# Kernel optimization log

Measured on AMD Instinct MI355X. Metric: run time of the kernel, lower is better.

## Reference

```python
import jax, jax.numpy as jnp
import numpy as np

BATCH, SEQ, DIM = 8, 2048, 512
NUM_Q, CODEBOOK = 8, 1024


def setup_inputs() -> dict:
    key = jax.random.key(0)
    k1, k2 = jax.random.split(key)
    x = jax.random.normal(k1, (BATCH, SEQ, DIM), dtype=jnp.float32)
    # one codebook per quantizer (uniform codebook size -> stacked [q, c, d])
    codebooks = jax.random.normal(k2, (NUM_Q, CODEBOOK, DIM), dtype=jnp.float32)
    return {"x": x, "codebooks": codebooks}


def reference(x, codebooks):
    """Residual VQ (Algorithm 1, SoundStream). Sequential nearest-neighbor
    quantization of the residual with straight-through estimator.
    project_in/project_out are Identity (codebook_dim == dim).
    Returns (quantized_out [b,n,d], indices [b,n,q], commit_losses [q]).
    """
    residual = x
    quantized_out = jnp.zeros_like(x)
    all_indices = []
    all_losses = []
    num_q = codebooks.shape[0]
    for q in range(num_q):  # small fixed loop over quantizer layers
        cb = codebooks[q]  # [c, d]
        # argmin of squared euclidean distance; ||r||^2 is constant over codes
        scores = -2.0 * jnp.einsum('bnd,cd->bnc', residual, cb) \
                 + jnp.sum(cb * cb, axis=-1)  # [b, n, c]
        idx = jnp.argmin(scores, axis=-1)  # [b, n]
        quant = cb[idx]  # gather codes: [b, n, d]
        # commitment loss (mse of detached quantize vs layer input)
        commit = jnp.mean((jax.lax.stop_gradient(quant) - residual) ** 2)
        # straight-through estimator
        quant_st = residual + jax.lax.stop_gradient(quant - residual)
        quantized_out = quantized_out + quant_st
        residual = residual - jax.lax.stop_gradient(quant)
        all_indices.append(idx)
        all_losses.append(commit)
    indices = jnp.stack(all_indices, axis=-1)  # [b, n, q]
    losses = jnp.stack(all_losses)  # [q]
    return quantized_out, indices, losses
```

## Files before the change

kernel.cpp:

```cpp
#include <hip/hip_runtime.h>
#include <cstdint>
#include <cstddef>


#define BATCH 8
#define SEQ   2048
#define DIM   512
#define NUMQ  8
#define CODES 1024
#define NPTS  (BATCH*SEQ)
#define MPTS  64
#define NWG   (NPTS/MPTS)
#define NTHR  512
#define NCHUNK 32
#define NCHUNK_TOT (NUMQ*NCHUNK)
#define CHUNK_BYTES 32768

#define OUT_IDX   (BATCH*SEQ*DIM)
#define OUT_LOSS  (OUT_IDX + BATCH*SEQ*NUMQ)

#define WS_LOSS   0
#define WS_CNORM  1024
#define WS_CBH    40960

typedef _Float16 f16x8  __attribute__((ext_vector_type(8)));
typedef _Float16 f16x4  __attribute__((ext_vector_type(4)));
typedef float    f32x16 __attribute__((ext_vector_type(16)));

__global__ void k_zero(double* loss) {
  if (threadIdx.x < NUMQ) loss[threadIdx.x] = 0.0;
}

__global__ void k_cnorm(const float* __restrict__ cb, float* __restrict__ cnorm) {
  int r = blockIdx.x * blockDim.x + threadIdx.x;
  const float* row = cb + (size_t)r * DIM;
  float s = 0.f;
  for (int d = 0; d < DIM; d += 4) {
    float4 v = *(const float4*)(row + d);
    s += v.x * v.x + v.y * v.y + v.z * v.z + v.w * v.w;
  }
  cnorm[r] = s;
}

__global__ void k_prep(const float* __restrict__ cb, unsigned char* __restrict__ cbH) {
  unsigned u = blockIdx.x * blockDim.x + threadIdx.x;
  unsigned h  = u & 1;
  unsigned v  = u >> 1;
  unsigned c  = v & 127;
  unsigned g  = (v >> 7) & 1;
  unsigned w  = (v >> 8) & 7;
  unsigned ks = (v >> 11) & 31;
  unsigned q  = v >> 16;
  unsigned code = (w << 7) | c;
  unsigned k = ks * 16 + g * 8 + h * 4;
  float4 val = *(const float4*)(cb + ((size_t)((q << 10) | code)) * DIM + k);
  f16x4 o;
  o[0] = (_Float16)val.x; o[1] = (_Float16)val.y;
  o[2] = (_Float16)val.z; o[3] = (_Float16)val.w;
  *(f16x4*)(cbH + (size_t)u * 8) = o;
}

__device__ __forceinline__ void stage(const unsigned char* __restrict__ cbH, int n,
                                      unsigned char* slot, int w, int cl) {
  const unsigned char* src = cbH + (size_t)n * CHUNK_BYTES + (w << 12) + (cl << 4);
  #pragma unroll
  for (int i = 0; i < 4; ++i)
    __builtin_amdgcn_global_load_lds(
        (const __attribute__((address_space(1))) void*)(src + i * 1024),
        (__attribute__((address_space(3))) void*)(slot + i * 1024), 16, 0, 0);
}

__launch_bounds__(NTHR, 2)
__global__ void k_main(const float* __restrict__ x, const float* __restrict__ cb,
                       const unsigned char* __restrict__ cbH,
                       const float* __restrict__ cnorm,
                       double* __restrict__ lossAcc,
                       float* __restrict__ out)
{
  __shared__ __align__(16) unsigned char Af[MPTS * DIM * 2];
  __shared__ __align__(16) unsigned char Bs[8][2][4096];
  __shared__ float          s1w[MPTS][8];
  __shared__ unsigned short id1w[MPTS][8];
  __shared__ unsigned short cand[MPTS][8][4];
  __shared__ unsigned char  ccnt[MPTS][8];
  __shared__ float          gmA[MPTS];
  __shared__ int            win0A[MPTS];
  __shared__ unsigned short idxs[MPTS][NUMQ];
  __shared__ double         lred[8];

  const int tid = threadIdx.x;
  const int cl  = tid & 63;
  const int w   = tid >> 6;
  const int l31 = cl & 31;
  const int l5  = cl >> 5;
  const int wg  = blockIdx.x;

  const int rp = tid >> 3;
  const int rj = tid & 7;
  const size_t gp = (size_t)wg * MPTS + rp;
  float4 r4[16];
  {
    const float4* xr = (const float4*)(x + gp * DIM + rj * 64);
    #pragma unroll
    for (int i = 0; i < 16; ++i) r4[i] = xr[i];
  }

  unsigned char* mySlot = &Bs[w][0][0];
  const int bOff = l5 * 2048 + l31 * 16;

  stage(cbH, 0, mySlot, w, cl);
  stage(cbH, 1, mySlot + 4096, w, cl);

  for (int q = 0; q < NUMQ; ++q) {
    #pragma unroll
    for (int i = 0; i < 8; ++i) {
      float4 a = r4[2 * i], b = r4[2 * i + 1];
      f16x8 v;
      v[0] = (_Float16)a.x; v[1] = (_Float16)a.y; v[2] = (_Float16)a.z; v[3] = (_Float16)a.w;
      v[4] = (_Float16)b.x; v[5] = (_Float16)b.y; v[6] = (_Float16)b.z; v[7] = (_Float16)b.w;
      int sl = ((i << 3) | rj) ^ (rp & 31);
      *(f16x8*)(Af + rp * 1024 + (sl << 4)) = v;
    }
    __syncthreads();

    f32x16 acc[2][4];
    #pragma unroll
    for (int mt = 0; mt < 2; ++mt)
      #pragma unroll
      for (int nt = 0; nt < 4; ++nt)
        #pragma unroll
        for (int e = 0; e < 16; ++e) acc[mt][nt][e] = 0.0f;

    #pragma unroll 1
    for (int ks = 0; ks < NCHUNK; ++ks) {
      if (q == NUMQ - 1 && ks == NCHUNK - 1)
        asm volatile("s_waitcnt vmcnt(0)" ::: "memory");
      else
        asm volatile("s_waitcnt vmcnt(4)" ::: "memory");
      const unsigned char* bufp = mySlot + ((ks & 1) << 12);
      const int s5 = (ks << 1) | l5;
      const int sf = ((((s5 & 7) << 3) | (s5 >> 3)) ^ l31) << 4;
      f16x8 a0 = *(const f16x8*)(Af + l31 * 1024 + sf);
      f16x8 a1 = *(const f16x8*)(Af + 32768 + l31 * 1024 + sf);
      f16x8 b0 = *(const f16x8*)(bufp + bOff);
      f16x8 b1 = *(const f16x8*)(bufp + bOff + 512);
      f16x8 b2 = *(const f16x8*)(bufp + bOff + 1024);
      f16x8 b3 = *(const f16x8*)(bufp + bOff + 1536);
      __builtin_amdgcn_s_setprio(1);
      acc[0][0] = __builtin_amdgcn_mfma_f32_32x32x16_f16(a0, b0, acc[0][0], 0, 0, 0);
      acc[0][1] = __builtin_amdgcn_mfma_f32_32x32x16_f16(a0, b1, acc[0][1], 0, 0, 0);
      acc[0][2] = __builtin_amdgcn_mfma_f32_32x32x16_f16(a0, b2, acc[0][2], 0, 0, 0);
      acc[0][3] = __builtin_amdgcn_mfma_f32_32x32x16_f16(a0, b3, acc[0][3], 0, 0, 0);
      acc[1][0] = __builtin_amdgcn_mfma_f32_32x32x16_f16(a1, b0, acc[1][0], 0, 0, 0);
      acc[1][1] = __builtin_amdgcn_mfma_f32_32x32x16_f16(a1, b1, acc[1][1], 0, 0, 0);
      acc[1][2] = __builtin_amdgcn_mfma_f32_32x32x16_f16(a1, b2, acc[1][2], 0, 0, 0);
      acc[1][3] = __builtin_amdgcn_mfma_f32_32x32x16_f16(a1, b3, acc[1][3], 0, 0, 0);
      __builtin_amdgcn_s_setprio(0);
      asm volatile("s_waitcnt lgkmcnt(0)" ::: "memory");
      const int n = (q << 5) + ks + 2;
      if (n < NCHUNK_TOT) stage(cbH, n, mySlot + ((ks & 1) << 12), w, cl);
    }

    {
      const float* cnq = cnorm + (q << 10) + (w << 7) + l31;
      const float cn0 = cnq[0], cn1 = cnq[32], cn2 = cnq[64], cn3 = cnq[96];
      #pragma unroll
      for (int mt = 0; mt < 2; ++mt) {
        acc[mt][0] = acc[mt][0] * -2.0f + cn0;
        acc[mt][1] = acc[mt][1] * -2.0f + cn1;
        acc[mt][2] = acc[mt][2] * -2.0f + cn2;
        acc[mt][3] = acc[mt][3] * -2.0f + cn3;
      }
    }

    #pragma unroll
    for (int mt = 0; mt < 2; ++mt)
      #pragma unroll
      for (int r = 0; r < 16; ++r) {
        float s = acc[mt][0][r]; int bi = l31;
        if (acc[mt][1][r] < s) { s = acc[mt][1][r]; bi = 32 + l31; }
        if (acc[mt][2][r] < s) { s = acc[mt][2][r]; bi = 64 + l31; }
        if (acc[mt][3][r] < s) { s = acc[mt][3][r]; bi = 96 + l31; }
        #pragma unroll
        for (int m = 1; m < 32; m <<= 1) {
          float os = __shfl_xor(s, m); int ob = __shfl_xor(bi, m);
          if (os < s || (os == s && ob < bi)) { s = os; bi = ob; }
        }
        if (l31 == 0) {
          int p = mt * 32 + (r & 3) + 8 * (r >> 2) + 4 * l5;
          s1w[p][w] = s; id1w[p][w] = (unsigned short)bi;
        }
      }
    __syncthreads();

    if (tid < MPTS) {
      int p = tid;
      float bs = s1w[p][0]; int bi = id1w[p][0];
      #pragma unroll
      for (int ww = 1; ww < 8; ++ww) {
        float s = s1w[p][ww];
        if (s < bs) { bs = s; bi = ww * 128 + id1w[p][ww]; }
      }
      gmA[p] = bs; win0A[p] = bi;
    }
    __syncthreads();

    #pragma unroll
    for (int mt = 0; mt < 2; ++mt)
      #pragma unroll
      for (int r = 0; r < 16; ++r) {
        const int p0 = mt * 32 + (r & 3) + 8 * (r >> 2);
        const float g0 = gmA[p0], g1 = gmA[p0 + 4];
        const float lim0 = g0 + 1.5f + 1e-4f * fabsf(g0);
        const float lim1 = g1 + 1.5f + 1e-4f * fabsf(g1);
        const float lim = l5 ? lim1 : lim0;
        unsigned long long b0 = __ballot(acc[mt][0][r] <= lim);
        unsigned long long b1 = __ballot(acc[mt][1][r] <= lim);
        unsigned long long b2 = __ballot(acc[mt][2][r] <= lim);
        unsigned long long b3 = __ballot(acc[mt][3][r] <= lim);
        if (cl == 0 || cl == 32) {
          const int p = p0 + (cl >> 3);
          unsigned short* cd = &cand[p][w][0];
          unsigned m0 = (cl == 0) ? (unsigned)b0 : (unsigned)(b0 >> 32);
          unsigned m1 = (cl == 0) ? (unsigned)b1 : (unsigned)(b1 >> 32);
          unsigned m2 = (cl == 0) ? (unsigned)b2 : (unsigned)(b2 >> 32);
          unsigned m3 = (cl == 0) ? (unsigned)b3 : (unsigned)(b3 >> 32);
          int n = 0;
          while (m0 && n < 4) { int bt = __builtin_ctz(m0); m0 &= m0 - 1; cd[n++] = (unsigned short)(bt); }
          while (m1 && n < 4) { int bt = __builtin_ctz(m1); m1 &= m1 - 1; cd[n++] = (unsigned short)(32 + bt); }
          while (m2 && n < 4) { int bt = __builtin_ctz(m2); m2 &= m2 - 1; cd[n++] = (unsigned short)(64 + bt); }
          while (m3 && n < 4) { int bt = __builtin_ctz(m3); m3 &= m3 - 1; cd[n++] = (unsigned short)(96 + bt); }
          ccnt[p][w] = (unsigned char)n;
        }
      }
    __syncthreads();

    #pragma unroll 1
    for (int pp = 0; pp < 8; ++pp) {
      const int p = (w << 3) + pp;
      int tot = 0;
      #pragma unroll
      for (int ww = 0; ww < 8; ++ww) tot += ccnt[p][ww];
      int winner;
      if (tot <= 1) {
        winner = win0A[p];
      } else {
        const size_t gpp = (size_t)wg * MPTS + p;
        double bs = 1.0e300, bs2 = 1.0e300; int bi = 0x7FFFFFFF;
        #pragma unroll 1
        for (int ww = 0; ww < 8; ++ww) {
          const int nn = ccnt[p][ww];
          #pragma unroll 1
          for (int si = 0; si < nn; ++si) {
            const int cc = ww * 128 + cand[p][ww][si];
            const float4* cr = (const float4*)(cb + ((size_t)q * CODES + cc) * DIM + (cl & 7) * 64);
            double dt = 0.0, cs = 0.0;
            #pragma unroll
            for (int i = 0; i < 16; ++i) {
              float4 cv = cr[i];
              dt += (double)r4[i].x * cv.x + (double)r4[i].y * cv.y
                  + (double)r4[i].z * cv.z + (double)r4[i].w * cv.w;
              cs += (double)cv.x * cv.x + (double)cv.y * cv.y
                  + (double)cv.z * cv.z + (double)cv.w * cv.w;
            }
            #pragma unroll
            for (int m = 1; m < 8; m <<= 1) { dt += __shfl_xor(dt, m); cs += __shfl_xor(cs, m); }
            double dtb = __shfl(dt, pp * 8), csb = __shfl(cs, pp * 8);
            double s = -2.0 * dtb + csb;
            if (s < bs) { bs2 = bs; bs = s; bi = cc; }
            else if (s < bs2) { bs2 = s; }
          }
        }
        if (bs2 - bs <= 1e-3 + 1e-6 * fabs(bs)) {
          bs = 1.0e300; bi = 0x7FFFFFFF;
          const float4* xr2 = (const float4*)(x + gpp * DIM + (cl & 7) * 64);
          #pragma unroll 1
          for (int ww = 0; ww < 8; ++ww) {
            const int nn = ccnt[p][ww];
            #pragma unroll 1
            for (int si = 0; si < nn; ++si) {
              const int cc = ww * 128 + cand[p][ww][si];
              const float4* cr = (const float4*)(cb + ((size_t)q * CODES + cc) * DIM + (cl & 7) * 64);
              double dt = 0.0, cs = 0.0;
              #pragma unroll 1
              for (int i = 0; i < 16; ++i) {
                float4 xv = xr2[i];
                double rhx = xv.x, rhy = xv.y, rhz = xv.z, rhw = xv.w;
                #pragma unroll 1
                for (int t2 = 0; t2 < q; ++t2) {
                  const float4* qr = (const float4*)(cb + ((size_t)t2 * CODES + idxs[p][t2]) * DIM + (cl & 7) * 64);
                  float4 qv = qr[i];
                  rhx -= (double)qv.x; rhy -= (double)qv.y;
                  rhz -= (double)qv.z; rhw -= (double)qv.w;
                }
                float4 cv = cr[i];
                dt += rhx * cv.x + rhy * cv.y + rhz * cv.z + rhw * cv.w;
                cs += (double)cv.x * cv.x + (double)cv.y * cv.y
                    + (double)cv.z * cv.z + (double)cv.w * cv.w;
              }
              #pragma unroll
              for (int m = 1; m < 8; m <<= 1) { dt += __shfl_xor(dt, m); cs += __shfl_xor(cs, m); }
              double dtb = __shfl(dt, pp * 8), csb = __shfl(cs, pp * 8);
              double s = -2.0 * dtb + csb;
              if (s < bs || (s == bs && cc < bi)) { bs = s; bi = cc; }
            }
          }
        }
        winner = bi;
      }
      if (cl == 0) idxs[p][q] = (unsigned short)winner;
    }
    __syncthreads();

    {
      const int win = idxs[rp][q];
      const float4* cr = (const float4*)(cb + ((size_t)q * CODES + win) * DIM + rj * 64);
      double ls = 0.0;
      #pragma unroll
      for (int i = 0; i < 16; ++i) {
        float4 cv = cr[i];
        float dx = cv.x - r4[i].x, dy = cv.y - r4[i].y;
        float dz = cv.z - r4[i].z, dw = cv.w - r4[i].w;
        ls += (double)dx * dx + (double)dy * dy + (double)dz * dz + (double)dw * dw;
        r4[i].x -= cv.x; r4[i].y -= cv.y; r4[i].z -= cv.z; r4[i].w -= cv.w;
      }
      #pragma unroll
      for (int m = 1; m < 64; m <<= 1) ls += __shfl_xor(ls, m);
      if (cl == 0) lred[w] = ls;
      __syncthreads();
      if (tid == 0) {
        double t = lred[0] + lred[1] + lred[2] + lred[3]
                 + lred[4] + lred[5] + lred[6] + lred[7];
        atomicAdd(lossAcc + q, t);
      }
      __syncthreads();
    }
  }

  {
    const float4* xr = (const float4*)(x + gp * DIM + rj * 64);
    float4* orow = (float4*)(out + gp * DIM + rj * 64);
    #pragma unroll
    for (int i = 0; i < 16; ++i) {
      float4 xv = xr[i];
      float4 o;
      o.x = xv.x - r4[i].x; o.y = xv.y - r4[i].y;
      o.z = xv.z - r4[i].z; o.w = xv.w - r4[i].w;
      orow[i] = o;
    }
  }
  if (tid < MPTS) {
    float* ob = out + OUT_IDX + ((size_t)wg * MPTS + tid) * NUMQ;
    #pragma unroll
    for (int j = 0; j < NUMQ; ++j) ob[j] = (float)idxs[tid][j];
  }
}

__global__ void k_fin(const double* __restrict__ loss, float* __restrict__ out) {
  int t = threadIdx.x;
  if (t < NUMQ)
    out[OUT_LOSS + t] = (float)(loss[t] / (double)((size_t)BATCH * SEQ * DIM));
}

extern "C" void kernel_launch(void* const* d_in, const int* in_sizes, int n_in,
                              void* d_out, int out_size, void* d_ws, size_t ws_size,
                              hipStream_t stream) {
  (void)in_sizes; (void)n_in; (void)out_size; (void)ws_size;
  const float* x  = (const float*)d_in[0];
  const float* cb = (const float*)d_in[1];
  float* out = (float*)d_out;
  char* ws = (char*)d_ws;
  double* loss = (double*)(ws + WS_LOSS);
  float* cnorm = (float*)(ws + WS_CNORM);
  unsigned char* cbH = (unsigned char*)(ws + WS_CBH);

  k_zero<<<1, 64, 0, stream>>>(loss);
  k_cnorm<<<NUMQ * CODES / 256, 256, 0, stream>>>(cb, cnorm);
  k_prep<<<NUMQ * NCHUNK * CHUNK_BYTES / 8 / 256, 256, 0, stream>>>(cb, cbH);
  k_main<<<NWG, NTHR, 0, stream>>>(x, cb, cbH, cnorm, loss, out);
  k_fin<<<1, 64, 0, stream>>>(loss, out);
}
```

Baseline: 632.1 us.

## Halve points per workgroup, single-buffer codebook chunks, raise occupancy to four blocks

```diff
diff --git a/kernel.cpp b/kernel.cpp
--- a/kernel.cpp
+++ b/kernel.cpp
@@ -9,7 +9,7 @@
 #define NUMQ  8
 #define CODES 1024
 #define NPTS  (BATCH*SEQ)
-#define MPTS  64
+#define MPTS  32
 #define NWG   (NPTS/MPTS)
 #define NTHR  512
 #define NCHUNK 32
@@ -70,7 +70,7 @@
         (__attribute__((address_space(3))) void*)(slot + i * 1024), 16, 0, 0);
 }
 
-__launch_bounds__(NTHR, 2)
+__launch_bounds__(NTHR, 4)
 __global__ void k_main(const float* __restrict__ x, const float* __restrict__ cb,
                        const unsigned char* __restrict__ cbH,
                        const float* __restrict__ cnorm,
@@ -78,7 +78,7 @@
                        float* __restrict__ out)
 {
   __shared__ __align__(16) unsigned char Af[MPTS * DIM * 2];
-  __shared__ __align__(16) unsigned char Bs[8][2][4096];
+  __shared__ __align__(16) unsigned char Bs[8][4096];
   __shared__ float          s1w[MPTS][8];
   __shared__ unsigned short id1w[MPTS][8];
   __shared__ unsigned short cand[MPTS][8][4];
@@ -95,102 +95,86 @@
   const int l5  = cl >> 5;
   const int wg  = blockIdx.x;
 
-  const int rp = tid >> 3;
-  const int rj = tid & 7;
+  const int rp = tid >> 4;
+  const int rj = tid & 15;
   const size_t gp = (size_t)wg * MPTS + rp;
-  float4 r4[16];
+  float4 r4[8];
   {
-    const float4* xr = (const float4*)(x + gp * DIM + rj * 64);
-    #pragma unroll
-    for (int i = 0; i < 16; ++i) r4[i] = xr[i];
-  }
-
-  unsigned char* mySlot = &Bs[w][0][0];
+    const float4* xr = (const float4*)(x + gp * DIM + rj * 32);
+    #pragma unroll
+    for (int i = 0; i < 8; ++i) r4[i] = xr[i];
+  }
+
+  unsigned char* mySlot = &Bs[w][0];
   const int bOff = l5 * 2048 + l31 * 16;
 
   stage(cbH, 0, mySlot, w, cl);
-  stage(cbH, 1, mySlot + 4096, w, cl);
 
   for (int q = 0; q < NUMQ; ++q) {
     #pragma unroll
-    for (int i = 0; i < 8; ++i) {
+    for (int i = 0; i < 4; ++i) {
       float4 a = r4[2 * i], b = r4[2 * i + 1];
       f16x8 v;
       v[0] = (_Float16)a.x; v[1] = (_Float16)a.y; v[2] = (_Float16)a.z; v[3] = (_Float16)a.w;
       v[4] = (_Float16)b.x; v[5] = (_Float16)b.y; v[6] = (_Float16)b.z; v[7] = (_Float16)b.w;
-      int sl = ((i << 3) | rj) ^ (rp & 31);
+      const int s = rj * 4 + i;
+      const int sl = (((s & 7) << 3) | (s >> 3)) ^ (rp & 31);
       *(f16x8*)(Af + rp * 1024 + (sl << 4)) = v;
     }
     __syncthreads();
 
-    f32x16 acc[2][4];
-    #pragma unroll
-    for (int mt = 0; mt < 2; ++mt)
-      #pragma unroll
-      for (int nt = 0; nt < 4; ++nt)
-        #pragma unroll
-        for (int e = 0; e < 16; ++e) acc[mt][nt][e] = 0.0f;
+    f32x16 acc[4];
+    #pragma unroll
+    for (int nt = 0; nt < 4; ++nt)
+      #pragma unroll
+      for (int e = 0; e < 16; ++e) acc[nt][e] = 0.0f;
 
     #pragma unroll 1
     for (int ks = 0; ks < NCHUNK; ++ks) {
-      if (q == NUMQ - 1 && ks == NCHUNK - 1)
-        asm volatile("s_waitcnt vmcnt(0)" ::: "memory");
-      else
-        asm volatile("s_waitcnt vmcnt(4)" ::: "memory");
-      const unsigned char* bufp = mySlot + ((ks & 1) << 12);
+      asm volatile("s_waitcnt vmcnt(0)" ::: "memory");
       const int s5 = (ks << 1) | l5;
       const int sf = ((((s5 & 7) << 3) | (s5 >> 3)) ^ l31) << 4;
       f16x8 a0 = *(const f16x8*)(Af + l31 * 1024 + sf);
-      f16x8 a1 = *(const f16x8*)(Af + 32768 + l31 * 1024 + sf);
-      f16x8 b0 = *(const f16x8*)(bufp + bOff);
-      f16x8 b1 = *(const f16x8*)(bufp + bOff + 512);
-      f16x8 b2 = *(const f16x8*)(bufp + bOff + 1024);
-      f16x8 b3 = *(const f16x8*)(bufp + bOff + 1536);
+      f16x8 b0 = *(const f16x8*)(mySlot + bOff);
+      f16x8 b1 = *(const f16x8*)(mySlot + bOff + 512);
+      f16x8 b2 = *(const f16x8*)(mySlot + bOff + 1024);
+      f16x8 b3 = *(const f16x8*)(mySlot + bOff + 1536);
       __builtin_amdgcn_s_setprio(1);
-      acc[0][0] = __builtin_amdgcn_mfma_f32_32x32x16_f16(a0, b0, acc[0][0], 0, 0, 0);
-      acc[0][1] = __builtin_amdgcn_mfma_f32_32x32x16_f16(a0, b1, acc[0][1], 0, 0, 0);
-      acc[0][2] = __builtin_amdgcn_mfma_f32_32x32x16_f16(a0, b2, acc[0][2], 0, 0, 0);
-      acc[0][3] = __builtin_amdgcn_mfma_f32_32x32x16_f16(a0, b3, acc[0][3], 0, 0, 0);
-      acc[1][0] = __builtin_amdgcn_mfma_f32_32x32x16_f16(a1, b0, acc[1][0], 0, 0, 0);
-      acc[1][1] = __builtin_amdgcn_mfma_f32_32x32x16_f16(a1, b1, acc[1][1], 0, 0, 0);
-      acc[1][2] = __builtin_amdgcn_mfma_f32_32x32x16_f16(a1, b2, acc[1][2], 0, 0, 0);
-      acc[1][3] = __builtin_amdgcn_mfma_f32_32x32x16_f16(a1, b3, acc[1][3], 0, 0, 0);
+      acc[0] = __builtin_amdgcn_mfma_f32_32x32x16_f16(a0, b0, acc[0], 0, 0, 0);
+      acc[1] = __builtin_amdgcn_mfma_f32_32x32x16_f16(a0, b1, acc[1], 0, 0, 0);
+      acc[2] = __builtin_amdgcn_mfma_f32_32x32x16_f16(a0, b2, acc[2], 0, 0, 0);
+      acc[3] = __builtin_amdgcn_mfma_f32_32x32x16_f16(a0, b3, acc[3], 0, 0, 0);
       __builtin_amdgcn_s_setprio(0);
       asm volatile("s_waitcnt lgkmcnt(0)" ::: "memory");
-      const int n = (q << 5) + ks + 2;
-      if (n < NCHUNK_TOT) stage(cbH, n, mySlot + ((ks & 1) << 12), w, cl);
+      const int n = (q << 5) + ks + 1;
+      if (n < NCHUNK_TOT) stage(cbH, n, mySlot, w, cl);
     }
 
     {
       const float* cnq = cnorm + (q << 10) + (w << 7) + l31;
       const float cn0 = cnq[0], cn1 = cnq[32], cn2 = cnq[64], cn3 = cnq[96];
-      #pragma unroll
-      for (int mt = 0; mt < 2; ++mt) {
-        acc[mt][0] = acc[mt][0] * -2.0f + cn0;
-        acc[mt][1] = acc[mt][1] * -2.0f + cn1;
-        acc[mt][2] = acc[mt][2] * -2.0f + cn2;
-        acc[mt][3] = acc[mt][3] * -2.0f + cn3;
-      }
-    }
-
-    #pragma unroll
-    for (int mt = 0; mt < 2; ++mt)
-      #pragma unroll
-      for (int r = 0; r < 16; ++r) {
-        float s = acc[mt][0][r]; int bi = l31;
-        if (acc[mt][1][r] < s) { s = acc[mt][1][r]; bi = 32 + l31; }
-        if (acc[mt][2][r] < s) { s = acc[mt][2][r]; bi = 64 + l31; }
-        if (acc[mt][3][r] < s) { s = acc[mt][3][r]; bi = 96 + l31; }
-        #pragma unroll
-        for (int m = 1; m < 32; m <<= 1) {
-          float os = __shfl_xor(s, m); int ob = __shfl_xor(bi, m);
-          if (os < s || (os == s && ob < bi)) { s = os; bi = ob; }
-        }
-        if (l31 == 0) {
-          int p = mt * 32 + (r & 3) + 8 * (r >> 2) + 4 * l5;
-          s1w[p][w] = s; id1w[p][w] = (unsigned short)bi;
-        }
-      }
+      acc[0] = acc[0] * -2.0f + cn0;
+      acc[1] = acc[1] * -2.0f + cn1;
+      acc[2] = acc[2] * -2.0f + cn2;
+      acc[3] = acc[3] * -2.0f + cn3;
+    }
+
+    #pragma unroll
+    for (int r = 0; r < 16; ++r) {
+      float s = acc[0][r]; int bi = l31;
+      if (acc[1][r] < s) { s = acc[1][r]; bi = 32 + l31; }
+      if (acc[2][r] < s) { s = acc[2][r]; bi = 64 + l31; }
+      if (acc[3][r] < s) { s = acc[3][r]; bi = 96 + l31; }
+      #pragma unroll
+      for (int m = 1; m < 32; m <<= 1) {
+        float os = __shfl_xor(s, m); int ob = __shfl_xor(bi, m);
+        if (os < s || (os == s && ob < bi)) { s = os; bi = ob; }
+      }
+      if (l31 == 0) {
+        int p = (r & 3) + 8 * (r >> 2) + 4 * l5;
+        s1w[p][w] = s; id1w[p][w] = (unsigned short)bi;
+      }
+    }
     __syncthreads();
 
     if (tid < MPTS) {
@@ -206,38 +190,36 @@
     __syncthreads();
 
     #pragma unroll
-    for (int mt = 0; mt < 2; ++mt)
-      #pragma unroll
-      for (int r = 0; r < 16; ++r) {
-        const int p0 = mt * 32 + (r & 3) + 8 * (r >> 2);
-        const float g0 = gmA[p0], g1 = gmA[p0 + 4];
-        const float lim0 = g0 + 1.5f + 1e-4f * fabsf(g0);
-        const float lim1 = g1 + 1.5f + 1e-4f * fabsf(g1);
-        const float lim = l5 ? lim1 : lim0;
-        unsigned long long b0 = __ballot(acc[mt][0][r] <= lim);
-        unsigned long long b1 = __ballot(acc[mt][1][r] <= lim);
-        unsigned long long b2 = __ballot(acc[mt][2][r] <= lim);
-        unsigned long long b3 = __ballot(acc[mt][3][r] <= lim);
-        if (cl == 0 || cl == 32) {
-          const int p = p0 + (cl >> 3);
-          unsigned short* cd = &cand[p][w][0];
-          unsigned m0 = (cl == 0) ? (unsigned)b0 : (unsigned)(b0 >> 32);
-          unsigned m1 = (cl == 0) ? (unsigned)b1 : (unsigned)(b1 >> 32);
-          unsigned m2 = (cl == 0) ? (unsigned)b2 : (unsigned)(b2 >> 32);
-          unsigned m3 = (cl == 0) ? (unsigned)b3 : (unsigned)(b3 >> 32);
-          int n = 0;
-          while (m0 && n < 4) { int bt = __builtin_ctz(m0); m0 &= m0 - 1; cd[n++] = (unsigned short)(bt); }
-          while (m1 && n < 4) { int bt = __builtin_ctz(m1); m1 &= m1 - 1; cd[n++] = (unsigned short)(32 + bt); }
-          while (m2 && n < 4) { int bt = __builtin_ctz(m2); m2 &= m2 - 1; cd[n++] = (unsigned short)(64 + bt); }
-          while (m3 && n < 4) { int bt = __builtin_ctz(m3); m3 &= m3 - 1; cd[n++] = (unsigned short)(96 + bt); }
-          ccnt[p][w] = (unsigned char)n;
-        }
-      }
+    for (int r = 0; r < 16; ++r) {
+      const int p0 = (r & 3) + 8 * (r >> 2);
+      const float g0 = gmA[p0], g1 = gmA[p0 + 4];
+      const float lim0 = g0 + 1.5f + 1e-4f * fabsf(g0);
+      const float lim1 = g1 + 1.5f + 1e-4f * fabsf(g1);
+      const float lim = l5 ? lim1 : lim0;
+      unsigned long long b0 = __ballot(acc[0][r] <= lim);
+      unsigned long long b1 = __ballot(acc[1][r] <= lim);
+      unsigned long long b2 = __ballot(acc[2][r] <= lim);
+      unsigned long long b3 = __ballot(acc[3][r] <= lim);
+      if (cl == 0 || cl == 32) {
+        const int p = p0 + (cl >> 3);
+        unsigned short* cd = &cand[p][w][0];
+        unsigned m0 = (cl == 0) ? (unsigned)b0 : (unsigned)(b0 >> 32);
+        unsigned m1 = (cl == 0) ? (unsigned)b1 : (unsigned)(b1 >> 32);
+        unsigned m2 = (cl == 0) ? (unsigned)b2 : (unsigned)(b2 >> 32);
+        unsigned m3 = (cl == 0) ? (unsigned)b3 : (unsigned)(b3 >> 32);
+        int n = 0;
+        while (m0 && n < 4) { int bt = __builtin_ctz(m0); m0 &= m0 - 1; cd[n++] = (unsigned short)(bt); }
+        while (m1 && n < 4) { int bt = __builtin_ctz(m1); m1 &= m1 - 1; cd[n++] = (unsigned short)(32 + bt); }
+        while (m2 && n < 4) { int bt = __builtin_ctz(m2); m2 &= m2 - 1; cd[n++] = (unsigned short)(64 + bt); }
+        while (m3 && n < 4) { int bt = __builtin_ctz(m3); m3 &= m3 - 1; cd[n++] = (unsigned short)(96 + bt); }
+        ccnt[p][w] = (unsigned char)n;
+      }
+    }
     __syncthreads();
 
     #pragma unroll 1
-    for (int pp = 0; pp < 8; ++pp) {
-      const int p = (w << 3) + pp;
+    for (int pp = 0; pp < 4; ++pp) {
+      const int p = (w << 2) + pp;
       int tot = 0;
       #pragma unroll
       for (int ww = 0; ww < 8; ++ww) tot += ccnt[p][ww];
@@ -253,10 +235,10 @@
           #pragma unroll 1
           for (int si = 0; si < nn; ++si) {
             const int cc = ww * 128 + cand[p][ww][si];
-            const float4* cr = (const float4*)(cb + ((size_t)q * CODES + cc) * DIM + (cl & 7) * 64);
+            const float4* cr = (const float4*)(cb + ((size_t)q * CODES + cc) * DIM + (cl & 15) * 32);
             double dt = 0.0, cs = 0.0;
             #pragma unroll
-            for (int i = 0; i < 16; ++i) {
+            for (int i = 0; i < 8; ++i) {
               float4 cv = cr[i];
               dt += (double)r4[i].x * cv.x + (double)r4[i].y * cv.y
                   + (double)r4[i].z * cv.z + (double)r4[i].w * cv.w;
@@ -264,8 +246,8 @@
                   + (double)cv.z * cv.z + (double)cv.w * cv.w;
             }
             #pragma unroll
-            for (int m = 1; m < 8; m <<= 1) { dt += __shfl_xor(dt, m); cs += __shfl_xor(cs, m); }
-            double dtb = __shfl(dt, pp * 8), csb = __shfl(cs, pp * 8);
+            for (int m = 1; m < 16; m <<= 1) { dt += __shfl_xor(dt, m); cs += __shfl_xor(cs, m); }
+            double dtb = __shfl(dt, pp * 16), csb = __shfl(cs, pp * 16);
             double s = -2.0 * dtb + csb;
             if (s < bs) { bs2 = bs; bs = s; bi = cc; }
             else if (s < bs2) { bs2 = s; }
@@ -273,22 +255,22 @@
         }
         if (bs2 - bs <= 1e-3 + 1e-6 * fabs(bs)) {
           bs = 1.0e300; bi = 0x7FFFFFFF;
-          const float4* xr2 = (const float4*)(x + gpp * DIM + (cl & 7) * 64);
+          const float4* xr2 = (const float4*)(x + gpp * DIM + (cl & 15) * 32);
           #pragma unroll 1
           for (int ww = 0; ww < 8; ++ww) {
             const int nn = ccnt[p][ww];
             #pragma unroll 1
             for (int si = 0; si < nn; ++si) {
               const int cc = ww * 128 + cand[p][ww][si];
-              const float4* cr = (const float4*)(cb + ((size_t)q * CODES + cc) * DIM + (cl & 7) * 64);
+              const float4* cr = (const float4*)(cb + ((size_t)q * CODES + cc) * DIM + (cl & 15) * 32);
               double dt = 0.0, cs = 0.0;
               #pragma unroll 1
-              for (int i = 0; i < 16; ++i) {
+              for (int i = 0; i < 8; ++i) {
                 float4 xv = xr2[i];
                 double rhx = xv.x, rhy = xv.y, rhz = xv.z, rhw = xv.w;
                 #pragma unroll 1
                 for (int t2 = 0; t2 < q; ++t2) {
-                  const float4* qr = (const float4*)(cb + ((size_t)t2 * CODES + idxs[p][t2]) * DIM + (cl & 7) * 64);
+                  const float4* qr = (const float4*)(cb + ((size_t)t2 * CODES + idxs[p][t2]) * DIM + (cl & 15) * 32);
                   float4 qv = qr[i];
                   rhx -= (double)qv.x; rhy -= (double)qv.y;
                   rhz -= (double)qv.z; rhw -= (double)qv.w;
@@ -299,8 +281,8 @@
                     + (double)cv.z * cv.z + (double)cv.w * cv.w;
               }
               #pragma unroll
-              for (int m = 1; m < 8; m <<= 1) { dt += __shfl_xor(dt, m); cs += __shfl_xor(cs, m); }
-              double dtb = __shfl(dt, pp * 8), csb = __shfl(cs, pp * 8);
+              for (int m = 1; m < 16; m <<= 1) { dt += __shfl_xor(dt, m); cs += __shfl_xor(cs, m); }
+              double dtb = __shfl(dt, pp * 16), csb = __shfl(cs, pp * 16);
               double s = -2.0 * dtb + csb;
               if (s < bs || (s == bs && cc < bi)) { bs = s; bi = cc; }
             }
@@ -314,10 +296,10 @@
 
     {
       const int win = idxs[rp][q];
-      const float4* cr = (const float4*)(cb + ((size_t)q * CODES + win) * DIM + rj * 64);
+      const float4* cr = (const float4*)(cb + ((size_t)q * CODES + win) * DIM + rj * 32);
       double ls = 0.0;
       #pragma unroll
-      for (int i = 0; i < 16; ++i) {
+      for (int i = 0; i < 8; ++i) {
         float4 cv = cr[i];
         float dx = cv.x - r4[i].x, dy = cv.y - r4[i].y;
         float dz = cv.z - r4[i].z, dw = cv.w - r4[i].w;
@@ -338,10 +320,10 @@
   }
 
   {
-    const float4* xr = (const float4*)(x + gp * DIM + rj * 64);
-    float4* orow = (float4*)(out + gp * DIM + rj * 64);
-    #pragma unroll
-    for (int i = 0; i < 16; ++i) {
+    const float4* xr = (const float4*)(x + gp * DIM + rj * 32);
+    float4* orow = (float4*)(out + gp * DIM + rj * 32);
+    #pragma unroll
+    for (int i = 0; i < 8; ++i) {
       float4 xv = xr[i];
       float4 o;
       o.x = xv.x - r4[i].x; o.y = xv.y - r4[i].y;
```

After: 628.4 us. About the same (-0.6%).

## Load codebook fragments directly into registers instead of staging through LDS

Applied to the files above, without the earlier changes.

```diff
diff --git a/kernel.cpp b/kernel.cpp
--- a/kernel.cpp
+++ b/kernel.cpp
@@ -13,7 +13,6 @@
 #define NWG   (NPTS/MPTS)
 #define NTHR  512
 #define NCHUNK 32
-#define NCHUNK_TOT (NUMQ*NCHUNK)
 #define CHUNK_BYTES 32768
 
 #define OUT_IDX   (BATCH*SEQ*DIM)
@@ -60,14 +59,14 @@
   *(f16x4*)(cbH + (size_t)u * 8) = o;
 }
 
-__device__ __forceinline__ void stage(const unsigned char* __restrict__ cbH, int n,
-                                      unsigned char* slot, int w, int cl) {
-  const unsigned char* src = cbH + (size_t)n * CHUNK_BYTES + (w << 12) + (cl << 4);
-  #pragma unroll
-  for (int i = 0; i < 4; ++i)
-    __builtin_amdgcn_global_load_lds(
-        (const __attribute__((address_space(1))) void*)(src + i * 1024),
-        (__attribute__((address_space(3))) void*)(slot + i * 1024), 16, 0, 0);
+struct BF { f16x8 b0, b1, b2, b3; };
+__device__ __forceinline__ BF loadB(const unsigned char* __restrict__ p) {
+  BF r;
+  r.b0 = *(const f16x8*)(p);
+  r.b1 = *(const f16x8*)(p + 512);
+  r.b2 = *(const f16x8*)(p + 1024);
+  r.b3 = *(const f16x8*)(p + 1536);
+  return r;
 }
 
 __launch_bounds__(NTHR, 2)
@@ -78,7 +77,6 @@
                        float* __restrict__ out)
 {
   __shared__ __align__(16) unsigned char Af[MPTS * DIM * 2];
-  __shared__ __align__(16) unsigned char Bs[8][2][4096];
   __shared__ float          s1w[MPTS][8];
   __shared__ unsigned short id1w[MPTS][8];
   __shared__ unsigned short cand[MPTS][8][4];
@@ -105,13 +103,12 @@
     for (int i = 0; i < 16; ++i) r4[i] = xr[i];
   }
 
-  unsigned char* mySlot = &Bs[w][0][0];
-  const int bOff = l5 * 2048 + l31 * 16;
-
-  stage(cbH, 0, mySlot, w, cl);
-  stage(cbH, 1, mySlot + 4096, w, cl);
-
   for (int q = 0; q < NUMQ; ++q) {
+    const unsigned char* bq = cbH + ((size_t)q << 20) + (w << 12) + (l5 << 11) + (l31 << 4);
+
+    BF s0 = loadB(bq);
+    BF s1 = loadB(bq + CHUNK_BYTES);
+
     #pragma unroll
     for (int i = 0; i < 8; ++i) {
       float4 a = r4[2 * i], b = r4[2 * i + 1];
@@ -132,33 +129,43 @@
         for (int e = 0; e < 16; ++e) acc[mt][nt][e] = 0.0f;
 
     #pragma unroll 1
-    for (int ks = 0; ks < NCHUNK; ++ks) {
-      if (q == NUMQ - 1 && ks == NCHUNK - 1)
-        asm volatile("s_waitcnt vmcnt(0)" ::: "memory");
-      else
-        asm volatile("s_waitcnt vmcnt(4)" ::: "memory");
-      const unsigned char* bufp = mySlot + ((ks & 1) << 12);
-      const int s5 = (ks << 1) | l5;
-      const int sf = ((((s5 & 7) << 3) | (s5 >> 3)) ^ l31) << 4;
-      f16x8 a0 = *(const f16x8*)(Af + l31 * 1024 + sf);
-      f16x8 a1 = *(const f16x8*)(Af + 32768 + l31 * 1024 + sf);
-      f16x8 b0 = *(const f16x8*)(bufp + bOff);
-      f16x8 b1 = *(const f16x8*)(bufp + bOff + 512);
-      f16x8 b2 = *(const f16x8*)(bufp + bOff + 1024);
-      f16x8 b3 = *(const f16x8*)(bufp + bOff + 1536);
-      __builtin_amdgcn_s_setprio(1);
-      acc[0][0] = __builtin_amdgcn_mfma_f32_32x32x16_f16(a0, b0, acc[0][0], 0, 0, 0);
-      acc[0][1] = __builtin_amdgcn_mfma_f32_32x32x16_f16(a0, b1, acc[0][1], 0, 0, 0);
-      acc[0][2] = __builtin_amdgcn_mfma_f32_32x32x16_f16(a0, b2, acc[0][2], 0, 0, 0);
-      acc[0][3] = __builtin_amdgcn_mfma_f32_32x32x16_f16(a0, b3, acc[0][3], 0, 0, 0);
-      acc[1][0] = __builtin_amdgcn_mfma_f32_32x32x16_f16(a1, b0, acc[1][0], 0, 0, 0);
-      acc[1][1] = __builtin_amdgcn_mfma_f32_32x32x16_f16(a1, b1, acc[1][1], 0, 0, 0);
-      acc[1][2] = __builtin_amdgcn_mfma_f32_32x32x16_f16(a1, b2, acc[1][2], 0, 0, 0);
-      acc[1][3] = __builtin_amdgcn_mfma_f32_32x32x16_f16(a1, b3, acc[1][3], 0, 0, 0);
-      __builtin_amdgcn_s_setprio(0);
-      asm volatile("s_waitcnt lgkmcnt(0)" ::: "memory");
-      const int n = (q << 5) + ks + 2;
-      if (n < NCHUNK_TOT) stage(cbH, n, mySlot + ((ks & 1) << 12), w, cl);
+    for (int kk = 0; kk < 16; ++kk) {
+      const int ks = kk << 1;
+      {
+        const int s5 = (ks << 1) | l5;
+        const int sf = ((((s5 & 7) << 3) | (s5 >> 3)) ^ l31) << 4;
+        f16x8 a0 = *(const f16x8*)(Af + l31 * 1024 + sf);
+        f16x8 a1 = *(const f16x8*)(Af + 32768 + l31 * 1024 + sf);
+        __builtin_amdgcn_s_setprio(1);
+        acc[0][0] = __builtin_amdgcn_mfma_f32_32x32x16_f16(a0, s0.b0, acc[0][0], 0, 0, 0);
+        acc[0][1] = __builtin_amdgcn_mfma_f32_32x32x16_f16(a0, s0.b1, acc[0][1], 0, 0, 0);
+        acc[0][2] = __builtin_amdgcn_mfma_f32_32x32x16_f16(a0, s0.b2, acc[0][2], 0, 0, 0);
+        acc[0][3] = __builtin_amdgcn_mfma_f32_32x32x16_f16(a0, s0.b3, acc[0][3], 0, 0, 0);
+        acc[1][0] = __builtin_amdgcn_mfma_f32_32x32x16_f16(a1, s0.b0, acc[1][0], 0, 0, 0);
+        acc[1][1] = __builtin_amdgcn_mfma_f32_32x32x16_f16(a1, s0.b1, acc[1][1], 0, 0, 0);
+        acc[1][2] = __builtin_amdgcn_mfma_f32_32x32x16_f16(a1, s0.b2, acc[1][2], 0, 0, 0);
+        acc[1][3] = __builtin_amdgcn_mfma_f32_32x32x16_f16(a1, s0.b3, acc[1][3], 0, 0, 0);
+        __builtin_amdgcn_s_setprio(0);
+        if (ks + 2 < NCHUNK) s0 = loadB(bq + (size_t)(ks + 2) * CHUNK_BYTES);
+      }
+      {
+        const int ks1 = ks + 1;
+        const int s5 = (ks1 << 1) | l5;
+        const int sf = ((((s5 & 7) << 3) | (s5 >> 3)) ^ l31) << 4;
+        f16x8 a0 = *(const f16x8*)(Af + l31 * 1024 + sf);
+        f16x8 a1 = *(const f16x8*)(Af + 32768 + l31 * 1024 + sf);
+        __builtin_amdgcn_s_setprio(1);
+        acc[0][0] = __builtin_amdgcn_mfma_f32_32x32x16_f16(a0, s1.b0, acc[0][0], 0, 0, 0);
+        acc[0][1] = __builtin_amdgcn_mfma_f32_32x32x16_f16(a0, s1.b1, acc[0][1], 0, 0, 0);
+        acc[0][2] = __builtin_amdgcn_mfma_f32_32x32x16_f16(a0, s1.b2, acc[0][2], 0, 0, 0);
+        acc[0][3] = __builtin_amdgcn_mfma_f32_32x32x16_f16(a0, s1.b3, acc[0][3], 0, 0, 0);
+        acc[1][0] = __builtin_amdgcn_mfma_f32_32x32x16_f16(a1, s1.b0, acc[1][0], 0, 0, 0);
+        acc[1][1] = __builtin_amdgcn_mfma_f32_32x32x16_f16(a1, s1.b1, acc[1][1], 0, 0, 0);
+        acc[1][2] = __builtin_amdgcn_mfma_f32_32x32x16_f16(a1, s1.b2, acc[1][2], 0, 0, 0);
+        acc[1][3] = __builtin_amdgcn_mfma_f32_32x32x16_f16(a1, s1.b3, acc[1][3], 0, 0, 0);
+        __builtin_amdgcn_s_setprio(0);
+        if (ks1 + 2 < NCHUNK) s1 = loadB(bq + (size_t)(ks1 + 2) * CHUNK_BYTES);
+      }
     }
 
     {
```

Result: faster. 613.1 us (-3.0%).
